# Kernel optimization log

Hardware: AMD Instinct MI355X
Metric: run time of the kernel (lower is better)

## Reference

```python
import jax, jax.numpy as jnp
from jax import lax
import numpy as np

# Heaviside spike with surrogate gradient (sdyt ~ d/dx tanh(x)); fwd is exact.
@jax.custom_vjp
def spike(x):
    return (x > 0).astype(x.dtype)

def _spike_fwd(x):
    return (x > 0).astype(x.dtype), x

def _spike_bwd(x, g):
    t = jnp.tanh(x)
    return (g * (1.0 - t * t),)

spike.defvjp(_spike_fwd, _spike_bwd)

def dyt(x, alpha, gamma, beta):
    # Dynamic Tanh norm: gamma * tanh(alpha * x) + beta
    return gamma * jnp.tanh(alpha * x) + beta

def slstm_seq(x, Wih, Whh, bih, bhh, thr, c0, h0):
    """Sequential SLSTM (snntorch, reset_mechanism='none') over a full sequence.
    x: [B,S,D]; Wih:[4H,D]; Whh:[4H,H]. Returns spikes [B,S,H], final (c, h)."""
    xg = jnp.einsum('bsd,gd->bsg', x, Wih) + bih  # precompute input gates [B,S,4H]

    def step(carry, xg_t):
        c, h = carry
        g = xg_t + h @ Whh.T + bhh
        i, f, gg, o = jnp.split(g, 4, axis=-1)  # torch LSTMCell gate order
        c = jax.nn.sigmoid(f) * c + jax.nn.sigmoid(i) * jnp.tanh(gg)
        h = jax.nn.sigmoid(o) * jnp.tanh(c)
        spk = spike(h - thr)
        return (c, h), spk

    (c, h), spks = lax.scan(step, (c0, h0), jnp.swapaxes(xg, 0, 1))
    return jnp.swapaxes(spks, 0, 1), c, h


def setup_inputs() -> dict:
    key = jax.random.key(0)
    ks = jax.random.split(key, 16)
    B, S, H, V, L = 4, 256, 512, 32000, 2
    G = 4 * H
    sc = 0.02
    d = {}
    d['src'] = jax.random.randint(ks[0], (B, S), 0, V)
    d['tgt'] = jax.random.randint(ks[1], (B, S), 0, V)
    d['emb_enc'] = jax.random.normal(ks[2], (V, H), jnp.float32) * sc
    d['enc_norm_alpha'] = jnp.full((1,), 0.5, jnp.float32)
    d['enc_norm_gamma'] = jnp.ones((H,), jnp.float32)
    d['enc_norm_beta'] = jnp.zeros((H,), jnp.float32)
    d['enc_Wih'] = jax.random.normal(ks[3], (L, G, H), jnp.float32) * sc
    d['enc_Whh'] = jax.random.normal(ks[4], (L, G, H), jnp.float32) * sc
    d['enc_bih'] = jnp.zeros((L, G), jnp.float32)
    d['enc_bhh'] = jnp.zeros((L, G), jnp.float32)
    d['enc_thr'] = jnp.ones((L, H), jnp.float32)
    d['emb_dec'] = jax.random.normal(ks[5], (V, H), jnp.float32) * sc
    d['dec_norm_alpha'] = jnp.full((1,), 0.5, jnp.float32)
    d['dec_norm_gamma'] = jnp.ones((H,), jnp.float32)
    d['dec_norm_beta'] = jnp.zeros((H,), jnp.float32)
    d['dec_Wih'] = jax.random.normal(ks[6], (L, G, H), jnp.float32) * sc
    d['dec_Whh'] = jax.random.normal(ks[7], (L, G, H), jnp.float32) * sc
    d['dec_bih'] = jnp.zeros((L, G), jnp.float32)
    d['dec_bhh'] = jnp.zeros((L, G), jnp.float32)
    d['dec_thr'] = jnp.ones((L, H), jnp.float32)
    d['dec_fc_W'] = jax.random.normal(ks[8], (L, H, H), jnp.float32) * sc
    d['dec_fc_b'] = jnp.zeros((L, H), jnp.float32)
    d['dec_dyt_alpha'] = jnp.full((L,), 0.5, jnp.float32)
    d['dec_dyt_gamma'] = jnp.ones((L, H), jnp.float32)
    d['dec_dyt_beta'] = jnp.zeros((L, H), jnp.float32)
    d['out_W'] = jax.random.normal(ks[9], (V, H), jnp.float32) * sc
    d['out_b'] = jnp.zeros((V,), jnp.float32)
    return d


def reference(src, tgt, emb_enc, enc_norm_alpha, enc_norm_gamma, enc_norm_beta,
              enc_Wih, enc_Whh, enc_bih, enc_bhh, enc_thr,
              emb_dec, dec_norm_alpha, dec_norm_gamma, dec_norm_beta,
              dec_Wih, dec_Whh, dec_bih, dec_bhh, dec_thr,
              dec_fc_W, dec_fc_b, dec_dyt_alpha, dec_dyt_gamma, dec_dyt_beta,
              out_W, out_b):
    L, _, H = enc_Wih.shape[0], enc_Wih.shape[1], enc_Wih.shape[2]
    B = src.shape[0]
    PAD = 0
    c0 = jnp.zeros((B, H), emb_enc.dtype)
    h0 = jnp.zeros((B, H), emb_enc.dtype)

    # ---- Encoder (note: non-bidirectional path feeds `src` to every layer, as in source) ----
    e_enc = emb_enc.at[PAD].set(0.0)  # padding_idx row is zero
    src_e = dyt(e_enc[src], enc_norm_alpha, enc_norm_gamma, enc_norm_beta)  # [B,S,H]
    syns, mems = [], []
    for l in range(L):
        _, c, h = slstm_seq(src_e, enc_Wih[l], enc_Whh[l], enc_bih[l], enc_bhh[l],
                            enc_thr[l], c0, h0)
        syns.append(c)
        mems.append(h)

    # ---- Decoder ----
    e_dec = emb_dec.at[PAD].set(0.0)
    x = dyt(e_dec[tgt], dec_norm_alpha, dec_norm_gamma, dec_norm_beta)  # [B,S,H]
    for l in range(L):
        spks, _, _ = slstm_seq(x, dec_Wih[l], dec_Whh[l], dec_bih[l], dec_bhh[l],
                               dec_thr[l], syns[l], mems[l])
        y = jnp.einsum('bsh,oh->bso', spks, dec_fc_W[l]) + dec_fc_b[l]
        if l > 0:  # residual=i>0
            y = y + x
        x = dyt(y, dec_dyt_alpha[l], dec_dyt_gamma[l], dec_dyt_beta[l])

    return jnp.einsum('bsh,vh->bsv', x, out_W) + out_b  # [B,S,V] logits
```

## Files before the change

kernel.cpp:

```cpp
#include <hip/hip_runtime.h>
#include <cstddef>

#define S_LEN 256
#define H_DIM 512
#define B_SZ  4

__device__ __forceinline__ float sigf(float x) { return 1.0f / (1.0f + expf(-x)); }

__global__ void zero_kernel(float* __restrict__ p, int n4) {
  int i = blockIdx.x * blockDim.x + threadIdx.x;
  if (i < n4) ((float4*)p)[i] = make_float4(0.f, 0.f, 0.f, 0.f);
}

__global__ __launch_bounds__(128)
void embed_dyt(const int* __restrict__ idx, const float* __restrict__ E,
               const float* __restrict__ alpha_p, const float* __restrict__ gamma,
               const float* __restrict__ beta, float* __restrict__ out) {
  const int row = blockIdx.x;
  const int t4  = threadIdx.x * 4;
  const int id  = idx[row];
  const float al = alpha_p[0];
  float4 e = make_float4(0.f, 0.f, 0.f, 0.f);
  if (id != 0) e = *(const float4*)(E + (size_t)id * H_DIM + t4);
  const float4 g = *(const float4*)(gamma + t4);
  const float4 b = *(const float4*)(beta + t4);
  float4 o;
  o.x = g.x * tanhf(al * e.x) + b.x;
  o.y = g.y * tanhf(al * e.y) + b.y;
  o.z = g.z * tanhf(al * e.z) + b.z;
  o.w = g.w * tanhf(al * e.w) + b.w;
  *(float4*)(out + (size_t)row * H_DIM + t4) = o;
}

template<int EPI>
__global__ __launch_bounds__(256)
void gemm_nt(const float* __restrict__ A, const float* __restrict__ W,
             const float* __restrict__ bias, float* __restrict__ C,
             int N, int K) {
  __shared__ float As[8][132];
  __shared__ float Ws[8][132];
  const int bm = blockIdx.x * 128;
  const int bn = blockIdx.y * 128;
  const int tid = threadIdx.x;
  const int tx = tid & 15, ty = tid >> 4;
  float acc[8][8] = {};
  const int i4 = tid * 4;
  const int lm = i4 >> 3;
  const int lk = i4 & 7;
  const float* Arow = A + (size_t)(bm + lm) * K + lk;
  const float* Wrow = W + (size_t)(bn + lm) * K + lk;

  for (int k0 = 0; k0 < K; k0 += 8) {
    float4 va = *(const float4*)(Arow + k0);
    float4 vw = *(const float4*)(Wrow + k0);
    As[lk + 0][lm] = va.x; As[lk + 1][lm] = va.y; As[lk + 2][lm] = va.z; As[lk + 3][lm] = va.w;
    Ws[lk + 0][lm] = vw.x; Ws[lk + 1][lm] = vw.y; Ws[lk + 2][lm] = vw.z; Ws[lk + 3][lm] = vw.w;
    __syncthreads();
#pragma unroll
    for (int kk = 0; kk < 8; ++kk) {
      float a[8], w[8];
      *(float4*)(a)     = *(const float4*)&As[kk][ty * 4];
      *(float4*)(a + 4) = *(const float4*)&As[kk][64 + ty * 4];
      *(float4*)(w)     = *(const float4*)&Ws[kk][tx * 4];
      *(float4*)(w + 4) = *(const float4*)&Ws[kk][64 + tx * 4];
#pragma unroll
      for (int ii = 0; ii < 8; ++ii)
#pragma unroll
        for (int jj = 0; jj < 8; ++jj)
          acc[ii][jj] += a[ii] * w[jj];
    }
    __syncthreads();
  }

#pragma unroll
  for (int ii = 0; ii < 8; ++ii) {
    const int row = bm + ((ii < 4) ? (ty * 4 + ii) : (60 + ty * 4 + ii));
#pragma unroll
    for (int hf = 0; hf < 2; ++hf) {
      const int ncol = bn + hf * 64 + tx * 4;
      float4 v;
      v.x = acc[ii][hf * 4 + 0]; v.y = acc[ii][hf * 4 + 1];
      v.z = acc[ii][hf * 4 + 2]; v.w = acc[ii][hf * 4 + 3];
      const float4 bb = *(const float4*)(bias + ncol);
      v.x += bb.x; v.y += bb.y; v.z += bb.z; v.w += bb.w;
      *(float4*)(C + (size_t)row * N + ncol) = v;
    }
  }
}

struct StepInst {
  const float* xg;
  const float* Whh;
  const float* bhh;
  float* c;
  const float* h_in;
  float* h_out;
  int xg_stride;
};

__global__ __launch_bounds__(256)
void slstm_step(StepInst I0, StepInst I1, int t) {
  StepInst I = (blockIdx.x < 64) ? I0 : I1;
  const int blk = blockIdx.x & 63;
  const int c0 = blk * 8;
  __shared__ float hs[4 * H_DIM];
  __shared__ float gred[32][4];
  const int tid = threadIdx.x;
  {
    const float4* s4 = (const float4*)I.h_in;
    float4* d4 = (float4*)hs;
    d4[tid] = s4[tid];
    d4[tid + 256] = s4[tid + 256];
  }
  __syncthreads();
  const int lr = tid >> 3, kc = tid & 7;
  const int q = lr >> 3, ci = lr & 7;
  const int grow = q * H_DIM + c0 + ci;
  const float* wrow = I.Whh + (size_t)grow * H_DIM;
  float a0 = 0.f, a1 = 0.f, a2 = 0.f, a3 = 0.f;
#pragma unroll
  for (int it = 0; it < 16; ++it) {
    const int k = it * 32 + kc * 4;
    const float4 w  = *(const float4*)(wrow + k);
    const float4 h0 = *(const float4*)&hs[0 * H_DIM + k];
    const float4 h1 = *(const float4*)&hs[1 * H_DIM + k];
    const float4 h2 = *(const float4*)&hs[2 * H_DIM + k];
    const float4 h3 = *(const float4*)&hs[3 * H_DIM + k];
    a0 += w.x * h0.x + w.y * h0.y + w.z * h0.z + w.w * h0.w;
    a1 += w.x * h1.x + w.y * h1.y + w.z * h1.z + w.w * h1.w;
    a2 += w.x * h2.x + w.y * h2.y + w.z * h2.z + w.w * h2.w;
    a3 += w.x * h3.x + w.y * h3.y + w.z * h3.z + w.w * h3.w;
  }
#pragma unroll
  for (int off = 1; off < 8; off <<= 1) {
    a0 += __shfl_xor(a0, off);
    a1 += __shfl_xor(a1, off);
    a2 += __shfl_xor(a2, off);
    a3 += __shfl_xor(a3, off);
  }
  if (kc == 0) {
    const float bb = I.bhh[grow];
    gred[lr][0] = a0 + I.xg[(size_t)(0 * S_LEN + t) * I.xg_stride + grow] + bb;
    gred[lr][1] = a1 + I.xg[(size_t)(1 * S_LEN + t) * I.xg_stride + grow] + bb;
    gred[lr][2] = a2 + I.xg[(size_t)(2 * S_LEN + t) * I.xg_stride + grow] + bb;
    gred[lr][3] = a3 + I.xg[(size_t)(3 * S_LEN + t) * I.xg_stride + grow] + bb;
  }
  __syncthreads();
  if (tid < 32) {
    const int b = tid & 3, cc = tid >> 2;
    const int col = c0 + cc;
    const float gi = gred[cc][b];
    const float gf = gred[8 + cc][b];
    const float gg = gred[16 + cc][b];
    const float go = gred[24 + cc][b];
    const float cold = I.c[b * H_DIM + col];
    const float cn = sigf(gf) * cold + sigf(gi) * tanhf(gg);
    const float hn = sigf(go) * tanhf(cn);
    I.c[b * H_DIM + col] = cn;
    I.h_out[b * H_DIM + col] = hn;
  }
}

struct DecArgs {
  const float* xg0;
  float*       xg1;
  const float* Whh0; const float* Whh1;
  const float* bhh0; const float* bhh1;
  const float* Wih1; const float* bih1;
  const float* fc0W; const float* fc0b;
  const float* fc1W; const float* fc1b;
  const float* dyt_a;
  const float* dyt_g;
  const float* dyt_b;
  const float* thr0; const float* thr1;
  float* c0; float* c1;
  const float* h0_init; const float* h1_init;
  float* ring0; float* ring1;
  float* spk0; float* spk1;
  float* x1;  float* x2;
};

__device__ __forceinline__ void rec_step(
    int g, int t, int tid,
    const float* __restrict__ xg, const float* __restrict__ Whh,
    const float* __restrict__ bhh, const float* __restrict__ h_init,
    float* __restrict__ ring, float* __restrict__ c,
    float* __restrict__ spk, const float* __restrict__ thr,
    float* hs, float (*gred)[4]) {
  const float* h_in = (t == 0) ? h_init : (ring + (size_t)(t & 1) * 2048);
  float* h_out = ring + (size_t)((t + 1) & 1) * 2048;
  const int c0 = g * 8;
  {
    const float4* s4 = (const float4*)h_in;
    float4* d4 = (float4*)hs;
    d4[tid] = s4[tid];
    d4[tid + 256] = s4[tid + 256];
  }
  __syncthreads();
  const int lr = tid >> 3, kc = tid & 7;
  const int q = lr >> 3, ci = lr & 7;
  const int grow = q * H_DIM + c0 + ci;
  const float* wrow = Whh + (size_t)grow * H_DIM;
  float a0 = 0.f, a1 = 0.f, a2 = 0.f, a3 = 0.f;
#pragma unroll
  for (int it = 0; it < 16; ++it) {
    const int k = it * 32 + kc * 4;
    const float4 w  = *(const float4*)(wrow + k);
    const float4 h0 = *(const float4*)&hs[0 * H_DIM + k];
    const float4 h1 = *(const float4*)&hs[1 * H_DIM + k];
    const float4 h2 = *(const float4*)&hs[2 * H_DIM + k];
    const float4 h3 = *(const float4*)&hs[3 * H_DIM + k];
    a0 += w.x * h0.x + w.y * h0.y + w.z * h0.z + w.w * h0.w;
    a1 += w.x * h1.x + w.y * h1.y + w.z * h1.z + w.w * h1.w;
    a2 += w.x * h2.x + w.y * h2.y + w.z * h2.z + w.w * h2.w;
    a3 += w.x * h3.x + w.y * h3.y + w.z * h3.z + w.w * h3.w;
  }
#pragma unroll
  for (int off = 1; off < 8; off <<= 1) {
    a0 += __shfl_xor(a0, off);
    a1 += __shfl_xor(a1, off);
    a2 += __shfl_xor(a2, off);
    a3 += __shfl_xor(a3, off);
  }
  if (kc == 0) {
    const float bb = bhh[grow];
    gred[lr][0] = a0 + xg[(size_t)(0 * S_LEN + t) * 2048 + grow] + bb;
    gred[lr][1] = a1 + xg[(size_t)(1 * S_LEN + t) * 2048 + grow] + bb;
    gred[lr][2] = a2 + xg[(size_t)(2 * S_LEN + t) * 2048 + grow] + bb;
    gred[lr][3] = a3 + xg[(size_t)(3 * S_LEN + t) * 2048 + grow] + bb;
  }
  __syncthreads();
  if (tid < 32) {
    const int b = tid & 3, cc = tid >> 2;
    const int col = c0 + cc;
    const float gi = gred[cc][b];
    const float gf = gred[8 + cc][b];
    const float gg = gred[16 + cc][b];
    const float go = gred[24 + cc][b];
    const float cold = c[b * H_DIM + col];
    const float cn = sigf(gf) * cold + sigf(gi) * tanhf(gg);
    const float hn = sigf(go) * tanhf(cn);
    c[b * H_DIM + col] = cn;
    h_out[b * H_DIM + col] = hn;
    spk[(size_t)(b * S_LEN + t) * H_DIM + col] = (hn - thr[col]) > 0.f ? 1.f : 0.f;
  }
}

__device__ __forceinline__ void stage_rows(const float* __restrict__ src, int t,
                                           int tid, float* hs) {
  float4* d4 = (float4*)hs;
  const int f0 = tid, f1 = tid + 256;
  d4[f0] = *(const float4*)(src + (size_t)((f0 >> 7) * S_LEN + t) * H_DIM + (f0 & 127) * 4);
  d4[f1] = *(const float4*)(src + (size_t)((f1 >> 7) * S_LEN + t) * H_DIM + (f1 & 127) * 4);
}

__global__ __launch_bounds__(256)
void dec_slot(DecArgs A, int s) {
  __shared__ float hs[4 * H_DIM];
  __shared__ float gred[32][4];
  const int bid = blockIdx.x;
  const int tid = threadIdx.x;

  if (bid < 64) {
    const int t = s;
    if (t < 256)
      rec_step(bid, t, tid, A.xg0, A.Whh0, A.bhh0, A.h0_init, A.ring0, A.c0,
               A.spk0, A.thr0, hs, gred);
  } else if (bid < 128) {
    const int t = s - 3;
    if (t >= 0 && t < 256)
      rec_step(bid - 64, t, tid, A.xg1, A.Whh1, A.bhh1, A.h1_init, A.ring1, A.c1,
               A.spk1, A.thr1, hs, gred);
  } else if (bid < 192) {
    const int t = s - 2;
    if (t >= 0 && t < 256) {
      stage_rows(A.x1, t, tid, hs);
      __syncthreads();
      const int wc = bid - 128;
      const int lr = tid >> 3, kc = tid & 7;
      const int row = wc * 32 + lr;
      const float* wrow = A.Wih1 + (size_t)row * H_DIM;
      float a0 = 0.f, a1 = 0.f, a2 = 0.f, a3 = 0.f;
#pragma unroll
      for (int it = 0; it < 16; ++it) {
        const int k = it * 32 + kc * 4;
        const float4 w  = *(const float4*)(wrow + k);
        const float4 h0 = *(const float4*)&hs[0 * H_DIM + k];
        const float4 h1 = *(const float4*)&hs[1 * H_DIM + k];
        const float4 h2 = *(const float4*)&hs[2 * H_DIM + k];
        const float4 h3 = *(const float4*)&hs[3 * H_DIM + k];
        a0 += w.x * h0.x + w.y * h0.y + w.z * h0.z + w.w * h0.w;
        a1 += w.x * h1.x + w.y * h1.y + w.z * h1.z + w.w * h1.w;
        a2 += w.x * h2.x + w.y * h2.y + w.z * h2.z + w.w * h2.w;
        a3 += w.x * h3.x + w.y * h3.y + w.z * h3.z + w.w * h3.w;
      }
#pragma unroll
      for (int off = 1; off < 8; off <<= 1) {
        a0 += __shfl_xor(a0, off);
        a1 += __shfl_xor(a1, off);
        a2 += __shfl_xor(a2, off);
        a3 += __shfl_xor(a3, off);
      }
      if (kc == 0) {
        const float bb = A.bih1[row];
        A.xg1[(size_t)(0 * S_LEN + t) * 2048 + row] = a0 + bb;
        A.xg1[(size_t)(1 * S_LEN + t) * 2048 + row] = a1 + bb;
        A.xg1[(size_t)(2 * S_LEN + t) * 2048 + row] = a2 + bb;
        A.xg1[(size_t)(3 * S_LEN + t) * 2048 + row] = a3 + bb;
      }
    }
  } else {
    const bool isB = (bid < 224);
    const int t = isB ? (s - 1) : (s - 4);
    if (t >= 0 && t < 256) {
      const float* spk = isB ? A.spk0 : A.spk1;
      const float* fcW = isB ? A.fc0W : A.fc1W;
      const float* fcb = isB ? A.fc0b : A.fc1b;
      const int lidx = isB ? 0 : 1;
      float* outp = isB ? A.x1 : A.x2;
      stage_rows(spk, t, tid, hs);
      __syncthreads();
      const int wb = bid - (isB ? 192 : 224);
      const int lr = tid >> 4, kc = tid & 15;
      const int col = wb * 16 + lr;
      const float* wrow = fcW + (size_t)col * H_DIM;
      float a0 = 0.f, a1 = 0.f, a2 = 0.f, a3 = 0.f;
#pragma unroll
      for (int it = 0; it < 8; ++it) {
        const int k = kc * 32 + it * 4;
        const float4 w  = *(const float4*)(wrow + k);
        const float4 h0 = *(const float4*)&hs[0 * H_DIM + k];
        const float4 h1 = *(const float4*)&hs[1 * H_DIM + k];
        const float4 h2 = *(const float4*)&hs[2 * H_DIM + k];
        const float4 h3 = *(const float4*)&hs[3 * H_DIM + k];
        a0 += w.x * h0.x + w.y * h0.y + w.z * h0.z + w.w * h0.w;
        a1 += w.x * h1.x + w.y * h1.y + w.z * h1.z + w.w * h1.w;
        a2 += w.x * h2.x + w.y * h2.y + w.z * h2.z + w.w * h2.w;
        a3 += w.x * h3.x + w.y * h3.y + w.z * h3.z + w.w * h3.w;
      }
#pragma unroll
      for (int off = 1; off < 16; off <<= 1) {
        a0 += __shfl_xor(a0, off);
        a1 += __shfl_xor(a1, off);
        a2 += __shfl_xor(a2, off);
        a3 += __shfl_xor(a3, off);
      }
      if (kc == 0) {
        const float al = A.dyt_a[lidx];
        const float gm = A.dyt_g[lidx * H_DIM + col];
        const float be = A.dyt_b[lidx * H_DIM + col];
        const float bb = fcb[col];
        float v[4] = {a0, a1, a2, a3};
#pragma unroll
        for (int b = 0; b < 4; ++b) {
          float y = v[b] + bb;
          if (!isB) y += A.x1[(size_t)(b * S_LEN + t) * H_DIM + col];
          outp[(size_t)(b * S_LEN + t) * H_DIM + col] = gm * tanhf(al * y) + be;
        }
      }
    }
  }
}

extern "C" void kernel_launch(void* const* d_in, const int* in_sizes, int n_in,
                              void* d_out, int out_size, void* d_ws, size_t ws_size,
                              hipStream_t stream) {
  (void)in_sizes; (void)n_in; (void)out_size; (void)ws_size;
  const int*   src       = (const int*)d_in[0];
  const int*   tgt       = (const int*)d_in[1];
  const float* emb_enc   = (const float*)d_in[2];
  const float* enc_alpha = (const float*)d_in[3];
  const float* enc_gamma = (const float*)d_in[4];
  const float* enc_beta  = (const float*)d_in[5];
  const float* enc_Wih   = (const float*)d_in[6];
  const float* enc_Whh   = (const float*)d_in[7];
  const float* enc_bih   = (const float*)d_in[8];
  const float* enc_bhh   = (const float*)d_in[9];
  const float* emb_dec   = (const float*)d_in[11];
  const float* dec_alpha = (const float*)d_in[12];
  const float* dec_gamma = (const float*)d_in[13];
  const float* dec_beta  = (const float*)d_in[14];
  const float* dec_Wih   = (const float*)d_in[15];
  const float* dec_Whh   = (const float*)d_in[16];
  const float* dec_bih   = (const float*)d_in[17];
  const float* dec_bhh   = (const float*)d_in[18];
  const float* dec_thr   = (const float*)d_in[19];
  const float* dec_fc_W  = (const float*)d_in[20];
  const float* dec_fc_b  = (const float*)d_in[21];
  const float* dyt_alpha = (const float*)d_in[22];
  const float* dyt_gamma = (const float*)d_in[23];
  const float* dyt_beta  = (const float*)d_in[24];
  const float* out_W     = (const float*)d_in[25];
  const float* out_b     = (const float*)d_in[26];
  float* out = (float*)d_out;

  float* ws     = (float*)d_ws;
  float* src_e  = ws;
  float* dec_x0 = ws + 524288;
  float* x1     = ws + 1048576;
  float* x2     = ws + 1572864;
  float* xg_enc = ws + 2097152;
  float* xg_d0  = xg_enc;
  float* xg_d1  = xg_enc + 2097152;
  float* spk0   = ws + 6291456;
  float* spk1   = ws + 6815744;
  float* st     = ws + 7340032;
  float* zbuf    = st;
  float* c0buf   = st + 2048;
  float* c1buf   = st + 4096;
  float* ring_e0 = st + 6144;
  float* ring_e1 = st + 10240;
  float* ring_d0 = st + 14336;
  float* ring_d1 = st + 18432;

  zero_kernel<<<6, 256, 0, stream>>>(st, 1536);
  embed_dyt<<<1024, 128, 0, stream>>>(src, emb_enc, enc_alpha, enc_gamma, enc_beta, src_e);
  embed_dyt<<<1024, 128, 0, stream>>>(tgt, emb_dec, dec_alpha, dec_gamma, dec_beta, dec_x0);

  gemm_nt<0><<<dim3(8, 32), 256, 0, stream>>>(src_e, enc_Wih, enc_bih, xg_enc, 4096, 512);

  for (int t = 0; t < 256; ++t) {
    StepInst A, B;
    A.xg = xg_enc;        A.Whh = enc_Whh;            A.bhh = enc_bhh;
    A.c = c0buf;
    A.h_in  = (t == 0) ? zbuf : ring_e0 + (t & 1) * 2048;
    A.h_out = ring_e0 + ((t + 1) & 1) * 2048;
    A.xg_stride = 4096;
    B.xg = xg_enc + 2048; B.Whh = enc_Whh + 1048576;  B.bhh = enc_bhh + 2048;
    B.c = c1buf;
    B.h_in  = (t == 0) ? zbuf : ring_e1 + (t & 1) * 2048;
    B.h_out = ring_e1 + ((t + 1) & 1) * 2048;
    B.xg_stride = 4096;
    slstm_step<<<128, 256, 0, stream>>>(A, B, t);
  }

  gemm_nt<0><<<dim3(8, 16), 256, 0, stream>>>(dec_x0, dec_Wih, dec_bih, xg_d0, 2048, 512);

  DecArgs D;
  D.xg0 = xg_d0;              D.xg1 = xg_d1;
  D.Whh0 = dec_Whh;           D.Whh1 = dec_Whh + 1048576;
  D.bhh0 = dec_bhh;           D.bhh1 = dec_bhh + 2048;
  D.Wih1 = dec_Wih + 1048576; D.bih1 = dec_bih + 2048;
  D.fc0W = dec_fc_W;          D.fc0b = dec_fc_b;
  D.fc1W = dec_fc_W + 262144; D.fc1b = dec_fc_b + 512;
  D.dyt_a = dyt_alpha;        D.dyt_g = dyt_gamma;     D.dyt_b = dyt_beta;
  D.thr0 = dec_thr;           D.thr1 = dec_thr + 512;
  D.c0 = c0buf;               D.c1 = c1buf;
  D.h0_init = ring_e0;        D.h1_init = ring_e1;
  D.ring0 = ring_d0;          D.ring1 = ring_d1;
  D.spk0 = spk0;              D.spk1 = spk1;
  D.x1 = x1;                  D.x2 = x2;

  for (int s = 0; s < 260; ++s)
    dec_slot<<<256, 256, 0, stream>>>(D, s);

  gemm_nt<0><<<dim3(8, 250), 256, 0, stream>>>(x2, out_W, out_b, out, 32000, 512);
}
```

Measured before the change: 2.940 ms.

## Replace fp32 SIMT GEMMs with bf16 MFMA GEMM and bf16 activations

Replaces the fp32 outer-product GEMM with a bf16 MFMA kernel (16x16x32) using swizzled LDS tiles, converting weights to bf16 on the fly. Embedding outputs and the final decoder activations are now stored in bf16 to feed it. This targets the large vocabulary projection and the input-gate GEMMs. In exchange, matmul inputs lose precision, which may shift spike threshold decisions.

```diff
diff --git a/kernel.cpp b/kernel.cpp
--- a/kernel.cpp
+++ b/kernel.cpp
@@ -3,9 +3,18 @@
 
 #define S_LEN 256
 #define H_DIM 512
-#define B_SZ  4
+
+typedef __attribute__((ext_vector_type(8))) short bf16x8;
+typedef __attribute__((ext_vector_type(4))) float f32x4;
+typedef __attribute__((ext_vector_type(8))) unsigned short u16x8;
 
 __device__ __forceinline__ float sigf(float x) { return 1.0f / (1.0f + expf(-x)); }
+
+__device__ __forceinline__ unsigned short cvt_bf16(float f) {
+  unsigned u = __float_as_uint(f);
+  u += 0x7fffu + ((u >> 16) & 1u);
+  return (unsigned short)(u >> 16);
+}
 
 __global__ void zero_kernel(float* __restrict__ p, int n4) {
   int i = blockIdx.x * blockDim.x + threadIdx.x;
@@ -15,7 +24,7 @@
 __global__ __launch_bounds__(128)
 void embed_dyt(const int* __restrict__ idx, const float* __restrict__ E,
                const float* __restrict__ alpha_p, const float* __restrict__ gamma,
-               const float* __restrict__ beta, float* __restrict__ out) {
+               const float* __restrict__ beta, unsigned short* __restrict__ out) {
   const int row = blockIdx.x;
   const int t4  = threadIdx.x * 4;
   const int id  = idx[row];
@@ -24,66 +33,84 @@
   if (id != 0) e = *(const float4*)(E + (size_t)id * H_DIM + t4);
   const float4 g = *(const float4*)(gamma + t4);
   const float4 b = *(const float4*)(beta + t4);
-  float4 o;
-  o.x = g.x * tanhf(al * e.x) + b.x;
-  o.y = g.y * tanhf(al * e.y) + b.y;
-  o.z = g.z * tanhf(al * e.z) + b.z;
-  o.w = g.w * tanhf(al * e.w) + b.w;
-  *(float4*)(out + (size_t)row * H_DIM + t4) = o;
-}
-
-template<int EPI>
+  ushort4 o;
+  o.x = cvt_bf16(g.x * tanhf(al * e.x) + b.x);
+  o.y = cvt_bf16(g.y * tanhf(al * e.y) + b.y);
+  o.z = cvt_bf16(g.z * tanhf(al * e.z) + b.z);
+  o.w = cvt_bf16(g.w * tanhf(al * e.w) + b.w);
+  *(ushort4*)(out + (size_t)row * H_DIM + t4) = o;
+}
+
 __global__ __launch_bounds__(256)
-void gemm_nt(const float* __restrict__ A, const float* __restrict__ W,
-             const float* __restrict__ bias, float* __restrict__ C,
-             int N, int K) {
-  __shared__ float As[8][132];
-  __shared__ float Ws[8][132];
-  const int bm = blockIdx.x * 128;
-  const int bn = blockIdx.y * 128;
+void gemm_bt_bf16(const unsigned short* __restrict__ A,
+                  const float* __restrict__ Bf,
+                  const float* __restrict__ bias,
+                  float* __restrict__ C, int N, int K) {
+  __shared__ unsigned short As[128 * 64];
+  __shared__ unsigned short Bs[128 * 64];
   const int tid = threadIdx.x;
-  const int tx = tid & 15, ty = tid >> 4;
-  float acc[8][8] = {};
-  const int i4 = tid * 4;
-  const int lm = i4 >> 3;
-  const int lk = i4 & 7;
-  const float* Arow = A + (size_t)(bm + lm) * K + lk;
-  const float* Wrow = W + (size_t)(bn + lm) * K + lk;
-
-  for (int k0 = 0; k0 < K; k0 += 8) {
-    float4 va = *(const float4*)(Arow + k0);
-    float4 vw = *(const float4*)(Wrow + k0);
-    As[lk + 0][lm] = va.x; As[lk + 1][lm] = va.y; As[lk + 2][lm] = va.z; As[lk + 3][lm] = va.w;
-    Ws[lk + 0][lm] = vw.x; Ws[lk + 1][lm] = vw.y; Ws[lk + 2][lm] = vw.z; Ws[lk + 3][lm] = vw.w;
+  const int bm = blockIdx.x * 128, bn = blockIdx.y * 128;
+  const int lane = tid & 63;
+  const int wr = (tid >> 7) & 1, wc = (tid >> 6) & 1;
+  f32x4 acc[4][4] = {};
+
+  const int srow = tid >> 3;
+  const int ss   = tid & 7;
+
+  for (int k0 = 0; k0 < K; k0 += 64) {
     __syncthreads();
 #pragma unroll
-    for (int kk = 0; kk < 8; ++kk) {
-      float a[8], w[8];
-      *(float4*)(a)     = *(const float4*)&As[kk][ty * 4];
-      *(float4*)(a + 4) = *(const float4*)&As[kk][64 + ty * 4];
-      *(float4*)(w)     = *(const float4*)&Ws[kk][tx * 4];
-      *(float4*)(w + 4) = *(const float4*)&Ws[kk][64 + tx * 4];
-#pragma unroll
-      for (int ii = 0; ii < 8; ++ii)
-#pragma unroll
-        for (int jj = 0; jj < 8; ++jj)
-          acc[ii][jj] += a[ii] * w[jj];
+    for (int p = 0; p < 4; ++p) {
+      const int row = srow + p * 32;
+      const int ps = ss ^ (row & 7);
+      u16x8 va = *(const u16x8*)(A + (size_t)(bm + row) * K + k0 + ss * 8);
+      *(u16x8*)(As + row * 64 + ps * 8) = va;
+      const float* bp = Bf + (size_t)(bn + row) * K + k0 + ss * 8;
+      const float4 b0 = *(const float4*)(bp);
+      const float4 b1 = *(const float4*)(bp + 4);
+      u16x8 vb;
+      vb[0] = cvt_bf16(b0.x); vb[1] = cvt_bf16(b0.y);
+      vb[2] = cvt_bf16(b0.z); vb[3] = cvt_bf16(b0.w);
+      vb[4] = cvt_bf16(b1.x); vb[5] = cvt_bf16(b1.y);
+      vb[6] = cvt_bf16(b1.z); vb[7] = cvt_bf16(b1.w);
+      *(u16x8*)(Bs + row * 64 + ps * 8) = vb;
     }
     __syncthreads();
-  }
-
-#pragma unroll
-  for (int ii = 0; ii < 8; ++ii) {
-    const int row = bm + ((ii < 4) ? (ty * 4 + ii) : (60 + ty * 4 + ii));
-#pragma unroll
-    for (int hf = 0; hf < 2; ++hf) {
-      const int ncol = bn + hf * 64 + tx * 4;
-      float4 v;
-      v.x = acc[ii][hf * 4 + 0]; v.y = acc[ii][hf * 4 + 1];
-      v.z = acc[ii][hf * 4 + 2]; v.w = acc[ii][hf * 4 + 3];
-      const float4 bb = *(const float4*)(bias + ncol);
-      v.x += bb.x; v.y += bb.y; v.z += bb.z; v.w += bb.w;
-      *(float4*)(C + (size_t)row * N + ncol) = v;
+#pragma unroll
+    for (int ks = 0; ks < 2; ++ks) {
+      const int r16 = lane & 15;
+      const int kslot = ks * 4 + (lane >> 4);
+      bf16x8 af[4], bfr[4];
+#pragma unroll
+      for (int m = 0; m < 4; ++m) {
+        const int row = wr * 64 + m * 16 + r16;
+        af[m] = *(const bf16x8*)(As + row * 64 + (kslot ^ (row & 7)) * 8);
+      }
+#pragma unroll
+      for (int n = 0; n < 4; ++n) {
+        const int row = wc * 64 + n * 16 + r16;
+        bfr[n] = *(const bf16x8*)(Bs + row * 64 + (kslot ^ (row & 7)) * 8);
+      }
+#pragma unroll
+      for (int m = 0; m < 4; ++m)
+#pragma unroll
+        for (int n = 0; n < 4; ++n)
+          acc[m][n] = __builtin_amdgcn_mfma_f32_16x16x32_bf16(af[m], bfr[n],
+                                                              acc[m][n], 0, 0, 0);
+    }
+  }
+
+  const int r16 = lane & 15, rg = lane >> 4;
+#pragma unroll
+  for (int m = 0; m < 4; ++m) {
+#pragma unroll
+    for (int n = 0; n < 4; ++n) {
+      const int col = bn + wc * 64 + n * 16 + r16;
+      const float bb = bias[col];
+      const int rowb = bm + wr * 64 + m * 16 + rg * 4;
+#pragma unroll
+      for (int r = 0; r < 4; ++r)
+        C[(size_t)(rowb + r) * N + col] = acc[m][n][r] + bb;
     }
   }
 }
@@ -177,7 +204,8 @@
   const float* h0_init; const float* h1_init;
   float* ring0; float* ring1;
   float* spk0; float* spk1;
-  float* x1;  float* x2;
+  float* x1;
+  unsigned short* x2;
 };
 
 __device__ __forceinline__ void rec_step(
@@ -317,7 +345,6 @@
       const float* fcW = isB ? A.fc0W : A.fc1W;
       const float* fcb = isB ? A.fc0b : A.fc1b;
       const int lidx = isB ? 0 : 1;
-      float* outp = isB ? A.x1 : A.x2;
       stage_rows(spk, t, tid, hs);
       __syncthreads();
       const int wb = bid - (isB ? 192 : 224);
@@ -355,7 +382,9 @@
         for (int b = 0; b < 4; ++b) {
           float y = v[b] + bb;
           if (!isB) y += A.x1[(size_t)(b * S_LEN + t) * H_DIM + col];
-          outp[(size_t)(b * S_LEN + t) * H_DIM + col] = gm * tanhf(al * y) + be;
+          const float r = gm * tanhf(al * y) + be;
+          if (isB) A.x1[(size_t)(b * S_LEN + t) * H_DIM + col] = r;
+          else     A.x2[(size_t)(b * S_LEN + t) * H_DIM + col] = cvt_bf16(r);
         }
       }
     }
@@ -394,17 +423,17 @@
   const float* out_b     = (const float*)d_in[26];
   float* out = (float*)d_out;
 
-  float* ws     = (float*)d_ws;
-  float* src_e  = ws;
-  float* dec_x0 = ws + 524288;
-  float* x1     = ws + 1048576;
-  float* x2     = ws + 1572864;
-  float* xg_enc = ws + 2097152;
-  float* xg_d0  = xg_enc;
-  float* xg_d1  = xg_enc + 2097152;
-  float* spk0   = ws + 6291456;
-  float* spk1   = ws + 6815744;
-  float* st     = ws + 7340032;
+  float* ws = (float*)d_ws;
+  float*          x1        = ws;
+  float*          xg_enc    = ws + 524288;
+  float*          xg_d0     = xg_enc;
+  float*          xg_d1     = xg_enc + 2097152;
+  float*          spk0      = ws + 4718592;
+  float*          spk1      = ws + 5242880;
+  unsigned short* src_e_bf  = (unsigned short*)(ws + 5767168);
+  unsigned short* dec_x0_bf = (unsigned short*)(ws + 6029312);
+  unsigned short* x2_bf     = (unsigned short*)(ws + 6291456);
+  float* st = ws + 6553600;
   float* zbuf    = st;
   float* c0buf   = st + 2048;
   float* c1buf   = st + 4096;
@@ -414,10 +443,13 @@
   float* ring_d1 = st + 18432;
 
   zero_kernel<<<6, 256, 0, stream>>>(st, 1536);
-  embed_dyt<<<1024, 128, 0, stream>>>(src, emb_enc, enc_alpha, enc_gamma, enc_beta, src_e);
-  embed_dyt<<<1024, 128, 0, stream>>>(tgt, emb_dec, dec_alpha, dec_gamma, dec_beta, dec_x0);
-
-  gemm_nt<0><<<dim3(8, 32), 256, 0, stream>>>(src_e, enc_Wih, enc_bih, xg_enc, 4096, 512);
+  embed_dyt<<<1024, 128, 0, stream>>>(src, emb_enc, enc_alpha, enc_gamma, enc_beta,
+                                      src_e_bf);
+  embed_dyt<<<1024, 128, 0, stream>>>(tgt, emb_dec, dec_alpha, dec_gamma, dec_beta,
+                                      dec_x0_bf);
+
+  gemm_bt_bf16<<<dim3(8, 32), 256, 0, stream>>>(src_e_bf, enc_Wih, enc_bih,
+                                                xg_enc, 4096, 512);
 
   for (int t = 0; t < 256; ++t) {
     StepInst A, B;
@@ -434,7 +466,8 @@
     slstm_step<<<128, 256, 0, stream>>>(A, B, t);
   }
 
-  gemm_nt<0><<<dim3(8, 16), 256, 0, stream>>>(dec_x0, dec_Wih, dec_bih, xg_d0, 2048, 512);
+  gemm_bt_bf16<<<dim3(8, 16), 256, 0, stream>>>(dec_x0_bf, dec_Wih, dec_bih,
+                                                xg_d0, 2048, 512);
 
   DecArgs D;
   D.xg0 = xg_d0;              D.xg1 = xg_d1;
@@ -449,10 +482,11 @@
   D.h0_init = ring_e0;        D.h1_init = ring_e1;
   D.ring0 = ring_d0;          D.ring1 = ring_d1;
   D.spk0 = spk0;              D.spk1 = spk1;
-  D.x1 = x1;                  D.x2 = x2;
+  D.x1 = x1;                  D.x2 = x2_bf;
 
   for (int s = 0; s < 260; ++s)
     dec_slot<<<256, 256, 0, stream>>>(D, s);
 
-  gemm_nt<0><<<dim3(8, 250), 256, 0, stream>>>(x2, out_W, out_b, out, 32000, 512);
-}
+  gemm_bt_bf16<<<dim3(8, 250), 256, 0, stream>>>(x2_bf, out_W, out_b,
+                                                 out, 32000, 512);
+}
```

Measured after the change: 2.604 ms. -11.4%, faster.
